# Kernel tuning notes

Measured on AMD Instinct MI355X. Metric: run time of the kernel, lower is better.

Reference implementation:

```python
import jax, jax.numpy as jnp
import numpy as np
import math

B, S, H, NH, HD = 2, 2048, 4096, 32, 128  # batch, seq, hidden, heads, head_dim
ROPE_BASE = 10000.0


def setup_inputs() -> dict:
    key = jax.random.key(0)
    k1, k2 = jax.random.split(key)
    hidden_states = jax.random.normal(k1, (B, S, H), jnp.float32) * 0.02
    W_pack = jax.random.normal(k2, (3 * H, H), jnp.float32) * (1.0 / math.sqrt(H))
    position_ids = jnp.tile(jnp.arange(S, dtype=jnp.int64)[None, :], (B, 1))
    # 4D additive causal mask, as passed by HF Baichuan to this attention module
    causal = jnp.triu(jnp.full((S, S), -1e9, jnp.float32), 1)[None, None, :, :]
    return {"hidden_states": hidden_states, "W_pack": W_pack,
            "attention_mask": causal, "position_ids": position_ids}


def _rope(x, position_ids):
    # x: [B, S, NH, HD]; NeoX-style rotate-half RoPE over full head_dim
    half = HD // 2
    inv_freq = 1.0 / (ROPE_BASE ** (jnp.arange(half, dtype=jnp.float32) / half))
    ang = position_ids.astype(jnp.float32)[:, :, None] * inv_freq  # [B,S,half]
    cos = jnp.concatenate([jnp.cos(ang), jnp.cos(ang)], axis=-1)[:, :, None, :]
    sin = jnp.concatenate([jnp.sin(ang), jnp.sin(ang)], axis=-1)[:, :, None, :]
    x1, x2 = jnp.split(x, 2, axis=-1)
    x_rot = jnp.concatenate([-x2, x1], axis=-1)
    return x * cos + x_rot * sin


def reference(hidden_states, W_pack, attention_mask, position_ids):
    # fused QKV projection (W_pack has no bias in Baichuan)
    proj = hidden_states @ W_pack.T                      # [B,S,3H]
    q, k, v = jnp.split(proj, 3, axis=-1)
    q = q.reshape(B, S, NH, HD)
    k = k.reshape(B, S, NH, HD)
    v = v.reshape(B, S, NH, HD)
    q = _rope(q, position_ids)
    k = _rope(k, position_ids)
    # scaled dot-product attention
    scale = 1.0 / math.sqrt(HD)
    q = q.transpose(0, 2, 1, 3)  # [B,NH,S,HD]
    k = k.transpose(0, 2, 1, 3)
    v = v.transpose(0, 2, 1, 3)
    scores = jnp.einsum("bhqd,bhkd->bhqk", q, k) * scale + attention_mask
    probs = jax.nn.softmax(scores, axis=-1)
    ctx = jnp.einsum("bhqk,bhkd->bhqd", probs, v)        # [B,NH,S,HD]
    attn_output = ctx.transpose(0, 2, 1, 3).reshape(B, S, H)
    return attn_output
```

## Files before the change

kernel.cpp:

```cpp
#include <hip/hip_runtime.h>
#include <hip/hip_bf16.h>
#include <stdint.h>

typedef unsigned short u16;
typedef __attribute__((ext_vector_type(8))) short s16x8;
typedef __attribute__((ext_vector_type(8))) unsigned short u16x8;
typedef __attribute__((ext_vector_type(4))) unsigned short u16x4;
typedef __attribute__((ext_vector_type(4))) float fx4;
typedef __bf16 bf16x8 __attribute__((ext_vector_type(8)));

#define SEQ 2048
#define HID 4096
#define NHEAD 32
#define HDIM 128
#define P3H 12288
#define NKT 64

__device__ __forceinline__ u16 f2bf(float f) {
  unsigned u = __builtin_bit_cast(unsigned, f);
  u += 0x7fffu + ((u >> 16) & 1u);
  return (u16)(u >> 16);
}
__device__ __forceinline__ float bf2f(u16 h) {
  unsigned u = ((unsigned)h) << 16;
  return __builtin_bit_cast(float, u);
}
__device__ __forceinline__ void gload_lds16(const void* g, void* l) {
  __builtin_amdgcn_global_load_lds((const __attribute__((address_space(1))) void*)g,
                                   (__attribute__((address_space(3))) void*)l, 16, 0, 0);
}
__device__ __forceinline__ fx4 mfma16(s16x8 a, s16x8 b, fx4 c) {
  return __builtin_amdgcn_mfma_f32_16x16x32_bf16(
      __builtin_bit_cast(bf16x8, a), __builtin_bit_cast(bf16x8, b), c, 0, 0, 0);
}

__global__ void k_cvt2(const float* __restrict__ s0, u16* __restrict__ d0, int n0,
                       const float* __restrict__ s1, u16* __restrict__ d1, int n1) {
  int i = blockIdx.x * blockDim.x + threadIdx.x;
  const float* src; u16* dst;
  if (i < n0) { src = s0; dst = d0; }
  else        { src = s1; dst = d1; i -= n0; if (i >= n1) return; }
  float4 v = reinterpret_cast<const float4*>(src)[i];
  u16x4 o;
  o[0] = f2bf(v.x); o[1] = f2bf(v.y); o[2] = f2bf(v.z); o[3] = f2bf(v.w);
  reinterpret_cast<u16x4*>(dst)[i] = o;
}

__device__ __forceinline__ void stage_half(const u16* __restrict__ g, u16* l, int r0, int t) {
#pragma unroll
  for (int c = 0; c < 2; c++) {
    int row = r0 + c * 64 + (t >> 3);
    int blk = (t & 7) ^ ((t >> 3) & 7);
    gload_lds16(g + (size_t)row * HID + blk * 8, l + row * 64 + (t & 7) * 8);
  }
}

#define BAR_OPEN __builtin_amdgcn_s_barrier()
#define BAR_CLOSE do { __builtin_amdgcn_s_barrier(); __builtin_amdgcn_sched_barrier(0); } while (0)
#define LGKM0 do { asm volatile("s_waitcnt lgkmcnt(0)" ::: "memory"); \
                   __builtin_amdgcn_sched_barrier(0); } while (0)

#define LDA_QUAD(qm) do { \
  _Pragma("unroll") for (int mi = 0; mi < 4; mi++) \
  _Pragma("unroll") for (int ks = 0; ks < 2; ks++) { \
    int row = wrr + (qm) * 64 + mi * 16 + li; \
    aA[mi][ks] = *(const s16x8*)&Al[row * 64 + (((ks * 4 + lg) ^ (row & 7)) << 3)]; \
  } } while (0)

#define LDB_QUAD(qn) do { \
  _Pragma("unroll") for (int ni = 0; ni < 2; ni++) \
  _Pragma("unroll") for (int ks = 0; ks < 2; ks++) { \
    int row = wcc + (qn) * 32 + ni * 16 + li; \
    aB[qn][ni][ks] = *(const s16x8*)&Bl[row * 64 + (((ks * 4 + lg) ^ (row & 7)) << 3)]; \
  } } while (0)

#define MMA_QUAD(qm, qn) do { \
  _Pragma("unroll") for (int ks = 0; ks < 2; ks++) \
  _Pragma("unroll") for (int mi = 0; mi < 4; mi++) \
  _Pragma("unroll") for (int ni = 0; ni < 2; ni++) \
    acc[(qm) * 4 + mi][(qn) * 2 + ni] = \
        mfma16(aA[mi][ks], aB[qn][ni][ks], acc[(qm) * 4 + mi][(qn) * 2 + ni]); \
  } while (0)

#define LTIDX(c, r) (((c) << 8) + ((r) ^ (((c) & 31) << 3)))

__global__ void __launch_bounds__(512, 2) k_gemm_qkv(const u16* __restrict__ A,
                                                     const u16* __restrict__ W,
                                                     u16* __restrict__ qo,
                                                     u16* __restrict__ ko,
                                                     u16* __restrict__ vo,
                                                     const int* __restrict__ pos) {
  __shared__ u16 SM[2][2][256 * 64];
  const int t = threadIdx.x;
  const int lane = t & 63;
  const int w = t >> 6;
  const int li = lane & 15, lg = lane >> 4;
  const int wr = w >> 2, wc = w & 3;
  const int wrr = wr * 128, wcc = wc * 64;

  const int cpx = gridDim.x >> 3;
  const int swz = (blockIdx.x & 7) * cpx + (blockIdx.x >> 3);
  const int bm = swz / 48, bn = swz - bm * 48;
  const int m0 = bm * 256, n0 = bn * 256;

  const u16* Ag = A + (size_t)m0 * HID;
  const u16* Wg = W + (size_t)n0 * HID;

  fx4 acc[8][4];
#pragma unroll
  for (int i = 0; i < 8; i++)
#pragma unroll
    for (int j = 0; j < 4; j++) acc[i][j] = fx4{0.f, 0.f, 0.f, 0.f};
  s16x8 aA[4][2], aB[2][2][2];

  stage_half(Wg, &SM[0][1][0], 0, t);
  stage_half(Wg, &SM[0][1][0], 128, t);
  stage_half(Ag, &SM[0][0][0], 0, t);
  stage_half(Ag, &SM[0][0][0], 128, t);
  stage_half(Wg + 64, &SM[1][1][0], 0, t);
  stage_half(Wg + 64, &SM[1][1][0], 128, t);
  asm volatile("s_waitcnt vmcnt(4)" ::: "memory");
  BAR_CLOSE;

  for (int kt = 0; kt < NKT; kt++) {
    const int cur = kt & 1;
    u16* Al = &SM[cur][0][0];
    u16* Bl = &SM[cur][1][0];
    u16* Anxt = &SM[cur ^ 1][0][0];
    const u16* Agn = Ag + (size_t)(kt + 1) * 64;
    const u16* Wgn = Wg + (size_t)(kt + 2) * 64;

    LDA_QUAD(0);
    LDB_QUAD(0);
    if (kt + 1 < NKT) stage_half(Agn, Anxt, 0, t);
    asm volatile("s_waitcnt lgkmcnt(8)" ::: "memory");
    BAR_OPEN;
    LGKM0;
    __builtin_amdgcn_s_setprio(1);
    MMA_QUAD(0, 0);
    __builtin_amdgcn_s_setprio(0);
    BAR_CLOSE;

    LDB_QUAD(1);
    if (kt + 1 < NKT) stage_half(Agn, Anxt, 128, t);
    BAR_OPEN;
    LGKM0;
    __builtin_amdgcn_s_setprio(1);
    MMA_QUAD(0, 1);
    __builtin_amdgcn_s_setprio(0);
    BAR_CLOSE;

    LDA_QUAD(1);
    if (kt + 2 < NKT) stage_half(Wgn, Bl, 0, t);
    BAR_OPEN;
    LGKM0;
    __builtin_amdgcn_s_setprio(1);
    MMA_QUAD(1, 1);
    __builtin_amdgcn_s_setprio(0);
    BAR_CLOSE;

    if (kt + 2 < NKT) stage_half(Wgn, Bl, 128, t);
    BAR_OPEN;
    LGKM0;
    __builtin_amdgcn_s_setprio(1);
    MMA_QUAD(1, 0);
    __builtin_amdgcn_s_setprio(0);
    if (kt + 2 < NKT) {
      asm volatile("s_waitcnt vmcnt(4)" ::: "memory");
    } else {
      asm volatile("s_waitcnt vmcnt(0)" ::: "memory");
    }
    BAR_CLOSE;
  }

  u16* LT = &SM[0][0][0];

#pragma unroll
  for (int mi = 0; mi < 8; mi++)
#pragma unroll
    for (int ni = 0; ni < 4; ni++) {
      u16x4 pk;
#pragma unroll
      for (int j = 0; j < 4; j++) pk[j] = f2bf(acc[mi][ni][j]);
      int c = wcc + ni * 16 + li;
      int r0 = wrr + mi * 16 + lg * 4;
      *reinterpret_cast<u16x4*>(&LT[LTIDX(c, r0)]) = pk;
    }
  __syncthreads();

  const int ttype = n0 >> 12;
  const int h0 = (n0 & 4095) >> 7;
  const int bb = m0 >> 11;
  const int sB = m0 & 2047;

  if (ttype < 2) {
    u16* dst = (ttype == 0) ? qo : ko;
    const float LG2E4 = 0.2076205059304601f;
    float invf = exp2f(-(float)lane * LG2E4);
    for (int it = 0; it < 64; ++it) {
      int i = w * 64 + it;
      int hh = i & 1, r = i >> 1;
      float x1 = bf2f(LT[LTIDX(hh * 128 + lane, r)]);
      float x2 = bf2f(LT[LTIDX(hh * 128 + lane + 64, r)]);
      float p = (float)pos[m0 + r];
      float sn, cs;
      sincosf(p * invf, &sn, &cs);
      size_t base = ((size_t)(bb * NHEAD + h0 + hh) * SEQ + sB + r) * HDIM;
      dst[base + lane]      = f2bf(x1 * cs - x2 * sn);
      dst[base + lane + 64] = f2bf(x2 * cs + x1 * sn);
    }
  } else {
    for (int it = 0; it < 16; ++it) {
      int cp = w * 16 + it;
      int c = cp * 2 + (lane >> 5);
      int ch = lane & 31;
      u16x8 v = *reinterpret_cast<const u16x8*>(&LT[LTIDX(c, ch * 8)]);
      int hh = c >> 7, d = c & 127;
      size_t base = ((size_t)(bb * NHEAD + h0 + hh) * HDIM + d) * SEQ + sB;
      *reinterpret_cast<u16x8*>(&vo[base + ch * 8]) = v;
    }
  }
}

__device__ __forceinline__ void stage_kv(const u16* __restrict__ kp, const u16* __restrict__ vp,
                                         u16* ksl, u16* vsl, int kv0, int t) {
#pragma unroll
  for (int c = 0; c < 4; c++) {
    int row = c * 16 + (t >> 4);
    int cb = (t & 15) ^ (row & 7);
    gload_lds16(kp + (size_t)(kv0 + row) * HDIM + cb * 8, ksl + (size_t)(c * 256 + t) * 8);
  }
#pragma unroll
  for (int c = 0; c < 4; c++) {
    int row = c * 32 + (t >> 3);
    int cb = (t & 7) ^ (row & 7);
    gload_lds16(vp + (size_t)row * SEQ + kv0 + cb * 8, vsl + (size_t)(c * 256 + t) * 8);
  }
}

__global__ void __launch_bounds__(256, 2) k_attn(const u16* __restrict__ q,
                                                 const u16* __restrict__ k,
                                                 const u16* __restrict__ vt,
                                                 float* __restrict__ out) {
  __shared__ u16 Ks[2][64 * 128];
  __shared__ u16 Vs[2][128 * 64];
  __shared__ u16 Ps[4][2][16 * 64];
  const int t = threadIdx.x;
  const int w = t >> 6, lane = t & 63;
  const int li = lane & 15, lg = lane >> 4;
  const int bh = blockIdx.x;
  const int qb = gridDim.y - 1 - blockIdx.y;
  const int b = bh >> 5, h = bh & 31;
  const int qw = qb * 128 + w * 32;
  const u16* qp = q + (size_t)bh * SEQ * HDIM;
  const u16* kp = k + (size_t)bh * SEQ * HDIM;
  const u16* vp = vt + (size_t)bh * HDIM * SEQ;

  s16x8 bq[2][4];
#pragma unroll
  for (int g = 0; g < 2; g++)
#pragma unroll
    for (int kk = 0; kk < 4; kk++)
      bq[g][kk] = *reinterpret_cast<const s16x8*>(
          &qp[(size_t)(qw + g * 16 + li) * HDIM + kk * 32 + lg * 8]);

  fx4 Oacc[2][8];
#pragma unroll
  for (int g = 0; g < 2; g++)
#pragma unroll
    for (int nd = 0; nd < 8; nd++) Oacc[g][nd] = fx4{0.f, 0.f, 0.f, 0.f};
  float mrun[2] = {-1e30f, -1e30f}, lrun[2] = {0.f, 0.f};

  const float SC2 = 0.12752551286084110f;
  const float THR = 8.0f / SC2;
  const int nt = 2 * (qb + 1);
  const int psw = (li & 7) << 4;

  stage_kv(kp, vp, Ks[0], Vs[0], 0, t);

  for (int tk = 0; tk < nt; tk++) {
    const int cur = tk & 1;
    if (tk + 1 < nt) {
      stage_kv(kp, vp, Ks[cur ^ 1], Vs[cur ^ 1], (tk + 1) * 64, t);
      asm volatile("s_waitcnt vmcnt(8)" ::: "memory");
    } else {
      asm volatile("s_waitcnt vmcnt(0)" ::: "memory");
    }
    __builtin_amdgcn_s_barrier();

    const u16* Kc = Ks[cur];
    const u16* Vc = Vs[cur];
    const int kv0 = tk * 64;
    const bool diag = (tk >= 2 * qb);

    fx4 sc[2][4];
#pragma unroll
    for (int g = 0; g < 2; g++)
#pragma unroll
      for (int n = 0; n < 4; n++) sc[g][n] = fx4{0.f, 0.f, 0.f, 0.f};
    __builtin_amdgcn_s_setprio(1);
#pragma unroll
    for (int n = 0; n < 4; n++) {
      int r = n * 16 + li;
#pragma unroll
      for (int kk = 0; kk < 4; kk++) {
        s16x8 ak = *reinterpret_cast<const s16x8*>(
            &Kc[r * 128 + (((kk * 4 + lg) ^ (r & 7)) << 3)]);
        sc[0][n] = mfma16(ak, bq[0][kk], sc[0][n]);
        sc[1][n] = mfma16(ak, bq[1][kk], sc[1][n]);
      }
    }
    __builtin_amdgcn_s_setprio(0);

    if (diag) {
#pragma unroll
      for (int g = 0; g < 2; g++) {
        const int qg = qw + g * 16 + li;
#pragma unroll
        for (int n = 0; n < 4; n++)
#pragma unroll
          for (int j = 0; j < 4; j++) {
            int kvg = kv0 + n * 16 + lg * 4 + j;
            if (kvg > qg) sc[g][n][j] = -1e30f;
          }
      }
    }

    s16x8 ap[2][2];
#pragma unroll
    for (int g = 0; g < 2; g++) {
      float mn[4];
#pragma unroll
      for (int n = 0; n < 4; n++)
        mn[n] = fmaxf(fmaxf(sc[g][n][0], sc[g][n][1]), fmaxf(sc[g][n][2], sc[g][n][3]));
      float vmax = fmaxf(fmaxf(mn[0], mn[1]), fmaxf(mn[2], mn[3]));
      vmax = fmaxf(vmax, __shfl_xor(vmax, 16));
      vmax = fmaxf(vmax, __shfl_xor(vmax, 32));
      if (__any(vmax > mrun[g] + THR)) {
        float mnew = fmaxf(mrun[g], vmax);
        float al = exp2f((mrun[g] - mnew) * SC2);
        mrun[g] = mnew;
        lrun[g] *= al;
        float alj[4];
#pragma unroll
        for (int j = 0; j < 4; j++) alj[j] = __shfl(al, lg * 4 + j);
#pragma unroll
        for (int nd = 0; nd < 8; nd++)
#pragma unroll
          for (int j = 0; j < 4; j++) Oacc[g][nd][j] *= alj[j];
      }
      const float mS = mrun[g] * SC2;
      float ps[4];
#pragma unroll
      for (int n = 0; n < 4; n++) {
        u16x4 pk;
        float pv0 = exp2f(__builtin_fmaf(sc[g][n][0], SC2, -mS));
        float pv1 = exp2f(__builtin_fmaf(sc[g][n][1], SC2, -mS));
        float pv2 = exp2f(__builtin_fmaf(sc[g][n][2], SC2, -mS));
        float pv3 = exp2f(__builtin_fmaf(sc[g][n][3], SC2, -mS));
        pk[0] = __builtin_bit_cast(u16, __float2bfloat16(pv0));
        pk[1] = __builtin_bit_cast(u16, __float2bfloat16(pv1));
        pk[2] = __builtin_bit_cast(u16, __float2bfloat16(pv2));
        pk[3] = __builtin_bit_cast(u16, __float2bfloat16(pv3));
        ps[n] = (pv0 + pv1) + (pv2 + pv3);
        *reinterpret_cast<u16x4*>(
            &Ps[w][g][li * 64 + (((n * 32 + lg * 8) ^ psw) >> 1)]) = pk;
      }
      float psum = (ps[0] + ps[1]) + (ps[2] + ps[3]);
      psum += __shfl_xor(psum, 16);
      psum += __shfl_xor(psum, 32);
      lrun[g] += psum;
#pragma unroll
      for (int kvc = 0; kvc < 2; kvc++)
        ap[g][kvc] = *reinterpret_cast<const s16x8*>(
            &Ps[w][g][li * 64 + (((kvc * 64 + lg * 16) ^ psw) >> 1)]);
    }

    __builtin_amdgcn_s_setprio(1);
#pragma unroll
    for (int nd = 0; nd < 8; nd++) {
      int dr = nd * 16 + li;
#pragma unroll
      for (int kvc = 0; kvc < 2; kvc++) {
        s16x8 bv = *reinterpret_cast<const s16x8*>(
            &Vc[dr * 64 + (((kvc * 4 + lg) ^ (dr & 7)) << 3)]);
        Oacc[0][nd] = mfma16(ap[0][kvc], bv, Oacc[0][nd]);
        Oacc[1][nd] = mfma16(ap[1][kvc], bv, Oacc[1][nd]);
      }
    }
    __builtin_amdgcn_s_setprio(0);

    __builtin_amdgcn_s_barrier();
    __builtin_amdgcn_sched_barrier(0);
  }

#pragma unroll
  for (int g = 0; g < 2; g++)
#pragma unroll
    for (int j = 0; j < 4; j++) {
      float rl = 1.0f / __shfl(lrun[g], lg * 4 + j);
      int s = qw + g * 16 + lg * 4 + j;
      float* op = out + ((size_t)(b * SEQ) + s) * HID + h * HDIM;
#pragma unroll
      for (int nd = 0; nd < 8; nd++) op[nd * 16 + li] = Oacc[g][nd][j] * rl;
    }
}

extern "C" void kernel_launch(void* const* d_in, const int* in_sizes, int n_in,
                              void* d_out, int out_size, void* d_ws, size_t ws_size,
                              hipStream_t stream) {
  const float* hidden = (const float*)d_in[0];
  const float* wpack = (const float*)d_in[1];
  const int* pos = (const int*)d_in[3];
  float* out = (float*)d_out;

  char* ws = (char*)d_ws;
  u16* hid_bf = (u16*)ws;
  u16* wp_bf = (u16*)(ws + ((size_t)32 << 20));
  u16* qb = (u16*)(ws + ((size_t)128 << 20));
  u16* kb = (u16*)(ws + ((size_t)160 << 20));
  u16* vtb = (u16*)(ws + ((size_t)192 << 20));

  const int n4h = HID * HID / 4, n4w = P3H * HID / 4;
  k_cvt2<<<(n4h + n4w + 255) / 256, 256, 0, stream>>>(hidden, hid_bf, n4h, wpack, wp_bf, n4w);

  k_gemm_qkv<<<768, 512, 0, stream>>>(hid_bf, wp_bf, qb, kb, vtb, pos);

  dim3 ga(2 * NHEAD, SEQ / 128);
  k_attn<<<ga, 256, 0, stream>>>(qb, kb, vtb, out);
}
```

Baseline: 544.1 us.

## Apply RoPE directly from MFMA accumulators by remapping wave column ownership

Each wave's B-tile columns are remapped so that it holds both halves (d and d+64) of the same head dimension pairs in registers. RoPE is then applied straight from the accumulators, with no round trip through LDS and no barrier for the Q and K tiles. The sin and cos are computed with the hardware sin/cos intrinsics on a range-reduced revolution count instead of sincosf. In exchange, the global stores become scattered 2-byte writes, which are less coalesced than before, and the hardware sin/cos intrinsics may be slightly less accurate.

```diff
diff --git a/kernel.cpp b/kernel.cpp
--- a/kernel.cpp
+++ b/kernel.cpp
@@ -68,10 +68,10 @@
   } } while (0)
 
 #define LDB_QUAD(qn) do { \
-  _Pragma("unroll") for (int ni = 0; ni < 2; ni++) \
+  _Pragma("unroll") for (int nn = 0; nn < 2; nn++) \
   _Pragma("unroll") for (int ks = 0; ks < 2; ks++) { \
-    int row = wcc + (qn) * 32 + ni * 16 + li; \
-    aB[qn][ni][ks] = *(const s16x8*)&Bl[row * 64 + (((ks * 4 + lg) ^ (row & 7)) << 3)]; \
+    int row = hh2 * 128 + qq2 * 32 + (qn) * 64 + nn * 16 + li; \
+    aB[qn][nn][ks] = *(const s16x8*)&Bl[row * 64 + (((ks * 4 + lg) ^ (row & 7)) << 3)]; \
   } } while (0)
 
 #define MMA_QUAD(qm, qn) do { \
@@ -96,7 +96,8 @@
   const int w = t >> 6;
   const int li = lane & 15, lg = lane >> 4;
   const int wr = w >> 2, wc = w & 3;
-  const int wrr = wr * 128, wcc = wc * 64;
+  const int wrr = wr * 128;
+  const int hh2 = wc >> 1, qq2 = wc & 1;
 
   const int cpx = gridDim.x >> 3;
   const int swz = (blockIdx.x & 7) * cpx + (blockIdx.x >> 3);
@@ -173,21 +174,6 @@
     BAR_CLOSE;
   }
 
-  u16* LT = &SM[0][0][0];
-
-#pragma unroll
-  for (int mi = 0; mi < 8; mi++)
-#pragma unroll
-    for (int ni = 0; ni < 4; ni++) {
-      u16x4 pk;
-#pragma unroll
-      for (int j = 0; j < 4; j++) pk[j] = f2bf(acc[mi][ni][j]);
-      int c = wcc + ni * 16 + li;
-      int r0 = wrr + mi * 16 + lg * 4;
-      *reinterpret_cast<u16x4*>(&LT[LTIDX(c, r0)]) = pk;
-    }
-  __syncthreads();
-
   const int ttype = n0 >> 12;
   const int h0 = (n0 & 4095) >> 7;
   const int bb = m0 >> 11;
@@ -196,20 +182,43 @@
   if (ttype < 2) {
     u16* dst = (ttype == 0) ? qo : ko;
     const float LG2E4 = 0.2076205059304601f;
-    float invf = exp2f(-(float)lane * LG2E4);
-    for (int it = 0; it < 64; ++it) {
-      int i = w * 64 + it;
-      int hh = i & 1, r = i >> 1;
-      float x1 = bf2f(LT[LTIDX(hh * 128 + lane, r)]);
-      float x2 = bf2f(LT[LTIDX(hh * 128 + lane + 64, r)]);
-      float p = (float)pos[m0 + r];
-      float sn, cs;
-      sincosf(p * invf, &sn, &cs);
-      size_t base = ((size_t)(bb * NHEAD + h0 + hh) * SEQ + sB + r) * HDIM;
-      dst[base + lane]      = f2bf(x1 * cs - x2 * sn);
-      dst[base + lane + 64] = f2bf(x2 * cs + x1 * sn);
+    const float LG2_2PI = 2.6514961294723187f;
+#pragma unroll
+    for (int p = 0; p < 2; p++) {
+      int d = qq2 * 32 + p * 16 + li;
+      float invf2 = exp2f(__builtin_fmaf(-(float)d, LG2E4, -LG2_2PI));
+#pragma unroll
+      for (int mi = 0; mi < 8; mi++) {
+        int r0 = wrr + mi * 16 + lg * 4;
+        int4 p4 = *reinterpret_cast<const int4*>(&pos[m0 + r0]);
+#pragma unroll
+        for (int j = 0; j < 4; j++) {
+          float pv = (float)((j == 0) ? p4.x : (j == 1) ? p4.y : (j == 2) ? p4.z : p4.w);
+          float rev = pv * invf2;
+          rev -= floorf(rev);
+          float sn = __builtin_amdgcn_sinf(rev);
+          float cs = __builtin_amdgcn_cosf(rev);
+          float x1 = acc[mi][p][j], x2 = acc[mi][p + 2][j];
+          size_t base = ((size_t)(bb * NHEAD + h0 + hh2) * SEQ + sB + r0 + j) * HDIM;
+          dst[base + d]      = f2bf(x1 * cs - x2 * sn);
+          dst[base + d + 64] = f2bf(x2 * cs + x1 * sn);
+        }
+      }
     }
   } else {
+    u16* LT = &SM[0][0][0];
+#pragma unroll
+    for (int mi = 0; mi < 8; mi++)
+#pragma unroll
+      for (int c2 = 0; c2 < 4; c2++) {
+        u16x4 pk;
+#pragma unroll
+        for (int j = 0; j < 4; j++) pk[j] = f2bf(acc[mi][c2][j]);
+        int c = hh2 * 128 + qq2 * 32 + (c2 >> 1) * 64 + (c2 & 1) * 16 + li;
+        int r0 = wrr + mi * 16 + lg * 4;
+        *reinterpret_cast<u16x4*>(&LT[LTIDX(c, r0)]) = pk;
+      }
+    __syncthreads();
     for (int it = 0; it < 16; ++it) {
       int cp = w * 16 + it;
       int c = cp * 2 + (lane >> 5);
```

New measurement: 533.0 us, median of 2. 2.1% less time.
